# Optimization experiments

Hardware: AMD Instinct MI355X
Metric: run time of the kernel (lower is better)

Reference implementation:

```python
import jax, jax.numpy as jnp
import numpy as np
import math

B, N = 16, 32            # batch, num_agents
D_OBS = 128              # obs_input_dim
N_ACT = 16               # num_actions
D_OA_IN = D_OBS + N_ACT  # obs_act_input_dim = 144
D_OUT = 128              # obs_output_dim == obs_act_output_dim
HID = 64                 # final hidden
FINAL_OUT = 1


def _xavier(k, shape):
    fan_out, fan_in = shape
    lim = math.sqrt(6.0 / (fan_in + fan_out))
    return jax.random.uniform(k, shape, jnp.float32, -lim, lim)


def setup_inputs() -> dict:
    key = jax.random.key(0)
    ks = jax.random.split(key, 12)
    return {
        "states": jax.random.normal(ks[0], (B, N, D_OBS), jnp.float32),
        "policies": jax.random.uniform(ks[1], (B, N, N_ACT), jnp.float32),
        "actions": jax.random.uniform(ks[2], (B, N, N_ACT), jnp.float32),
        # uniform noise in [0,1); forward applies (noise-0.5)*0.1 like torch.rand path
        "noise": jax.random.uniform(ks[3], (B, N, N, N, D_OUT), jnp.float32),
        # torch Linear weights: [out_features, in_features], bias=False
        "Wk_oa": _xavier(ks[4], (D_OUT, D_OA_IN)),
        "Wq_oa": _xavier(ks[5], (D_OUT, D_OA_IN)),
        "Wv_oa": _xavier(ks[6], (D_OUT, D_OA_IN)),
        "Wk_o": _xavier(ks[7], (D_OUT, D_OBS)),
        "Wq_o": _xavier(ks[8], (D_OUT, D_OBS)),
        "Wv_o": _xavier(ks[9], (D_OUT, D_OBS)),
        "W1": _xavier(ks[10], (HID, 2 * D_OUT)),
        "W2": _xavier(ks[11], (FINAL_OUT, HID)),
    }


def reference(states, policies, actions, noise, Wk_oa, Wq_oa, Wv_oa, Wk_o, Wq_o, Wv_o, W1, W2):
    n = states.shape[1]
    d_oa = Wk_oa.shape[0]
    d_o = Wk_o.shape[0]

    obs_actions = jnp.concatenate([states, actions], axis=-1)   # [B,N,D_oa_in]
    obs_policy = jnp.concatenate([states, policies], axis=-1)

    # --- obs-action attention branch ---
    K = obs_actions @ Wk_oa.T                                   # [B,N,d]
    Q = obs_actions @ Wq_oa.T
    # bmm(Q,K^T).transpose(1,2): score_t[b,j,i] = Q_i . K_j; softmax over i
    score_t = jnp.einsum('bid,bjd->bji', Q, K)
    w_oa = jax.nn.softmax(score_t / jnp.sqrt(jnp.asarray(d_oa, states.dtype)), axis=-1)  # [B,N,N]

    # place_policies/place_actions: diagonal picks obs_policy, off-diag obs_actions
    eye = jnp.eye(n, dtype=states.dtype)[None, :, :, None]       # [1,N,N,1]
    oap = eye * obs_policy[:, None, :, :] + (1.0 - eye) * obs_actions[:, None, :, :]  # [B,N,N,D_oa_in]
    AV = oap @ Wv_oa.T                                           # [B,N,N,d]

    # mean_i( AV[b,j,i,:] * w_oa[b,k,i] + (noise-0.5)*0.1 ); mean is linear -> split
    noise_mean = jnp.mean((noise - 0.5) * 0.1, axis=-2)          # [B,N,N,d]
    wav = jnp.einsum('bjid,bki->bkjd', AV, w_oa) / n + noise_mean  # [B,N,N,d]

    # --- obs-only attention branch ---
    Ko = states @ Wk_o.T
    Qo = states @ Wq_o.T
    AVO = states @ Wv_o.T                                        # [B,N,d]
    score_o = jnp.einsum('bid,bjd->bji', Qo, Ko)
    w_o = jax.nn.softmax(score_o / jnp.sqrt(jnp.asarray(d_o, states.dtype)), axis=-1)  # [B,N,N]
    wfo = jnp.einsum('bji,bid->bjd', w_o, AVO) / n               # [B,N,d]
    wfo_b = jnp.broadcast_to(wfo[:, :, None, :], wav.shape[:3] + (d_o,))  # [B,N,N,d]

    node = jnp.concatenate([wfo_b, wav], axis=-1)                # [B,N,N,2d]
    h = jax.nn.leaky_relu(node @ W1.T, negative_slope=0.01)
    value = h @ W2.T                                             # [B,N,N,1]
    return (value, w_oa, w_o[..., None])
```

## Files before the change

### kernel.cpp

```cpp
#include <hip/hip_runtime.h>


#define WS_K    0
#define WS_Q    65536
#define WS_VA   131072
#define WS_KO   196608
#define WS_QO   262144
#define WS_AVO  327680
#define WS_SDIV 393216
#define WS_DDIV 458752
#define WS_U    524288
#define WS_WOA  557056

__global__ __launch_bounds__(256) void k_transforms(
    const float* __restrict__ states, const float* __restrict__ policies,
    const float* __restrict__ actions,
    const float* __restrict__ Wk_oa, const float* __restrict__ Wq_oa,
    const float* __restrict__ Wv_oa, const float* __restrict__ Wk_o,
    const float* __restrict__ Wq_o,  const float* __restrict__ Wv_o,
    float* __restrict__ ws)
{
    __shared__ __align__(16) float xa[144];
    const int row = blockIdx.x;
    const int t = threadIdx.x;
    if (t < 128)       xa[t] = states[row * 128 + t];
    else if (t < 144)  xa[t] = actions[row * 16 + (t - 128)];
    __syncthreads();

    for (int u = t; u < 768; u += 256) {
        const int m = u >> 7, o = u & 127;
        const float* Wrow; int len4; float* dst;
        switch (m) {
            case 0: Wrow = Wk_oa + o * 144; len4 = 36; dst = ws + WS_K;  break;
            case 1: Wrow = Wq_oa + o * 144; len4 = 36; dst = ws + WS_Q;  break;
            case 2: Wrow = Wv_oa + o * 144; len4 = 36; dst = ws + WS_VA; break;
            case 3: Wrow = Wk_o  + o * 128; len4 = 32; dst = ws + WS_KO; break;
            case 4: Wrow = Wq_o  + o * 128; len4 = 32; dst = ws + WS_QO; break;
            default:Wrow = Wv_o  + o * 128; len4 = 32; dst = ws + WS_AVO;break;
        }
        const float4* W4 = (const float4*)Wrow;
        const float4* x4 = (const float4*)xa;
        float acc = 0.f;
        for (int c = 0; c < len4; ++c) {
            float4 w = W4[c], x = x4[c];
            acc += w.x * x.x + w.y * x.y + w.z * x.z + w.w * x.w;
        }
        dst[row * 128 + o] = acc;
    }
}

__global__ __launch_bounds__(256) void k_attn(
    const float* __restrict__ policies, const float* __restrict__ actions,
    const float* __restrict__ Wv_oa, const float* __restrict__ W1,
    float* __restrict__ ws, float* __restrict__ out)
{
    const float* K   = ws + WS_K;
    const float* Q   = ws + WS_Q;
    const float* Va  = ws + WS_VA;
    const float* Ko  = ws + WS_KO;
    const float* Qo  = ws + WS_QO;
    const float* AVO = ws + WS_AVO;
    float* Sdiv = ws + WS_SDIV;
    float* Ddiv = ws + WS_DDIV;
    float* U    = ws + WS_U;
    float* Woa  = ws + WS_WOA;

    const int b = blockIdx.x >> 5, r = blockIdx.x & 31;
    const int t = threadIdx.x;
    const int br = b * 32 + r;

    __shared__ __align__(16) float kr[128], kor[128], wfo[128];
    __shared__ float sA[32], sO[32], woa[32], wo[32], pd[16];

    if (t < 128) { kr[t] = K[br * 128 + t]; kor[t] = Ko[br * 128 + t]; }
    else if (t < 144) {
        int c = t - 128;
        pd[c] = policies[br * 16 + c] - actions[br * 16 + c];
    }
    __syncthreads();

    {
        const int i = t >> 3, seg = t & 7;
        const float4* q4  = (const float4*)(Q  + (b * 32 + i) * 128) + seg * 4;
        const float4* qo4 = (const float4*)(Qo + (b * 32 + i) * 128) + seg * 4;
        const float4* k4  = (const float4*)kr  + seg * 4;
        const float4* ko4 = (const float4*)kor + seg * 4;
        float a0 = 0.f, a1 = 0.f;
        #pragma unroll
        for (int c = 0; c < 4; ++c) {
            float4 q = q4[c], kk = k4[c];
            a0 += q.x * kk.x + q.y * kk.y + q.z * kk.z + q.w * kk.w;
            float4 p = qo4[c], mm = ko4[c];
            a1 += p.x * mm.x + p.y * mm.y + p.z * mm.z + p.w * mm.w;
        }
        #pragma unroll
        for (int off = 1; off < 8; off <<= 1) {
            a0 += __shfl_xor(a0, off, 64);
            a1 += __shfl_xor(a1, off, 64);
        }
        if (seg == 0) {
            const float scale = 0.08838834764831845f;
            sA[i] = a0 * scale;
            sO[i] = a1 * scale;
        }
    }
    __syncthreads();

    if (t < 64) {
        const int i = t & 31;
        float s = (t < 32) ? sA[i] : sO[i];
        float m = s;
        #pragma unroll
        for (int off = 1; off < 32; off <<= 1) m = fmaxf(m, __shfl_xor(m, off, 64));
        float e = __expf(s - m);
        float sum = e;
        #pragma unroll
        for (int off = 1; off < 32; off <<= 1) sum += __shfl_xor(sum, off, 64);
        float w = e / sum;
        if (t < 32) { woa[i] = w; out[16384 + br * 32 + i] = w; Woa[br * 32 + i] = w; }
        else        { wo[i]  = w; out[32768 + br * 32 + i] = w; }
    }
    __syncthreads();

    {
        const int d = t & 127;
        const float* M  = (t < 128) ? Va  : AVO;
        const float* wp = (t < 128) ? woa : wo;
        float acc = 0.f;
        #pragma unroll 8
        for (int i = 0; i < 32; ++i) acc += wp[i] * M[(b * 32 + i) * 128 + d];
        if (t < 128) {
            Sdiv[br * 128 + d] = acc * (1.f / 32.f);
            const float4* wv4 = (const float4*)(Wv_oa + d * 144 + 128);
            float dv = 0.f;
            #pragma unroll
            for (int c = 0; c < 4; ++c) {
                float4 w = wv4[c];
                dv += w.x * pd[4*c] + w.y * pd[4*c+1] + w.z * pd[4*c+2] + w.w * pd[4*c+3];
            }
            Ddiv[br * 128 + d] = dv * (1.f / 32.f);
        } else {
            wfo[d] = acc * (1.f / 32.f);
        }
    }
    __syncthreads();

    {
        const int h = t >> 2, q = t & 3;
        const float4* w4 = (const float4*)(W1 + h * 256) + q * 8;
        const float4* f4 = (const float4*)wfo + q * 8;
        float acc = 0.f;
        #pragma unroll
        for (int c = 0; c < 8; ++c) {
            float4 w = w4[c], f = f4[c];
            acc += w.x * f.x + w.y * f.y + w.z * f.z + w.w * f.w;
        }
        acc += __shfl_xor(acc, 1, 64);
        acc += __shfl_xor(acc, 2, 64);
        if (q == 0) U[br * 64 + h] = acc;
    }
}

__global__ __launch_bounds__(256) void k_value(
    const float* __restrict__ noise, const float* __restrict__ ws,
    const float* __restrict__ W1, const float* __restrict__ W2,
    float* __restrict__ out)
{
    const float* Sdiv = ws + WS_SDIV;
    const float* Ddiv = ws + WS_DDIV;
    const float* U    = ws + WS_U;
    const float* Woa  = ws + WS_WOA;

    const int blk = blockIdx.x;
    const int b  = blk >> 6;
    const int k  = (blk >> 1) & 31;
    const int j0 = (blk & 1) * 16;
    const int t  = threadIdx.x;
    const int h  = t >> 2, q = t & 3;
    const int lane = t & 63, wv = t >> 6;
    const int bk = b * 32 + k;

    __shared__ __align__(16) float part[512];
    __shared__ __align__(16) float wav_s[4 * 36];
    __shared__ float sdiv_s[128];
    __shared__ float woa_s[16];
    __shared__ float wsum[4];

    float w1r[32];
    {
        const float4* p = (const float4*)(W1 + h * 256 + 128 + q * 32);
        #pragma unroll
        for (int c = 0; c < 8; ++c) {
            float4 v = p[c];
            w1r[4*c] = v.x; w1r[4*c+1] = v.y; w1r[4*c+2] = v.z; w1r[4*c+3] = v.w;
        }
    }
    const float u_h  = U[bk * 64 + h];
    const float w2_h = W2[h];
    if (t < 128) sdiv_s[t] = Sdiv[bk * 128 + t];
    if (t < 16)  woa_s[t]  = Woa[bk * 32 + j0 + t];
    __syncthreads();

    const float4* nbase = (const float4*)noise + (size_t)(bk * 32) * 1024;

    float4 n0, n1, n2, n3;
    {
        const float4* p = nbase + (size_t)j0 * 1024 + t;
        n0 = p[0]; n1 = p[256]; n2 = p[512]; n3 = p[768];
    }
    for (int jj = 0; jj < 16; ++jj) {
        const int j = j0 + jj;
        float4 m0{}, m1{}, m2{}, m3{};
        if (jj < 15) {
            const float4* p = nbase + (size_t)(j + 1) * 1024 + t;
            m0 = p[0]; m1 = p[256]; m2 = p[512]; m3 = p[768];
        }
        float s0 = n0.x + n1.x + n2.x + n3.x;
        float s1 = n0.y + n1.y + n2.y + n3.y;
        float s2 = n0.z + n1.z + n2.z + n3.z;
        float s3 = n0.w + n1.w + n2.w + n3.w;
        s0 += __shfl_xor(s0, 32, 64);
        s1 += __shfl_xor(s1, 32, 64);
        s2 += __shfl_xor(s2, 32, 64);
        s3 += __shfl_xor(s3, 32, 64);
        if (lane < 32) {
            float4 v; v.x = s0; v.y = s1; v.z = s2; v.w = s3;
            ((float4*)part)[wv * 32 + lane] = v;
        }
        __syncthreads();
        if (t < 128) {
            float ns = part[t] + part[128 + t] + part[256 + t] + part[384 + t];
            float dv = Ddiv[(b * 32 + j) * 128 + t];
            float w  = sdiv_s[t] + dv * woa_s[jj] + ns * (0.1f / 32.f) - 0.05f;
            wav_s[(t >> 5) * 36 + (t & 31)] = w;
        }
        __syncthreads();
        {
            const float4* wv4 = (const float4*)(wav_s + q * 36);
            float acc = 0.f;
            #pragma unroll
            for (int c = 0; c < 8; ++c) {
                float4 v = wv4[c];
                acc += w1r[4*c] * v.x + w1r[4*c+1] * v.y
                     + w1r[4*c+2] * v.z + w1r[4*c+3] * v.w;
            }
            acc += __shfl_xor(acc, 1, 64);
            acc += __shfl_xor(acc, 2, 64);
            float hv = u_h + acc;
            hv = (hv > 0.f) ? hv : 0.01f * hv;
            float vp = (q == 0) ? hv * w2_h : 0.f;
            #pragma unroll
            for (int off = 4; off < 64; off <<= 1) vp += __shfl_xor(vp, off, 64);
            if (lane == 0) wsum[wv] = vp;
        }
        __syncthreads();
        if (t == 0) out[bk * 32 + j] = wsum[0] + wsum[1] + wsum[2] + wsum[3];
        n0 = m0; n1 = m1; n2 = m2; n3 = m3;
    }
}

extern "C" void kernel_launch(void* const* d_in, const int* in_sizes, int n_in,
                              void* d_out, int out_size, void* d_ws, size_t ws_size,
                              hipStream_t stream) {
    const float* states   = (const float*)d_in[0];
    const float* policies = (const float*)d_in[1];
    const float* actions  = (const float*)d_in[2];
    const float* noise    = (const float*)d_in[3];
    const float* Wk_oa    = (const float*)d_in[4];
    const float* Wq_oa    = (const float*)d_in[5];
    const float* Wv_oa    = (const float*)d_in[6];
    const float* Wk_o     = (const float*)d_in[7];
    const float* Wq_o     = (const float*)d_in[8];
    const float* Wv_o     = (const float*)d_in[9];
    const float* W1       = (const float*)d_in[10];
    const float* W2       = (const float*)d_in[11];
    float* out = (float*)d_out;
    float* ws  = (float*)d_ws;

    k_transforms<<<512, 256, 0, stream>>>(states, policies, actions,
                                          Wk_oa, Wq_oa, Wv_oa, Wk_o, Wq_o, Wv_o, ws);
    k_attn<<<512, 256, 0, stream>>>(policies, actions, Wv_oa, W1, ws, out);
    k_value<<<1024, 256, 0, stream>>>(noise, ws, W1, W2, out);
}
```

Before: 416.6 us.

## Fold noise reduction into transform kernel and fuse attention with value head

The three-kernel pipeline becomes two. The first kernel runs the linear transforms, including the policy-action diagonal correction, and also reduces the noise tensor over its reduction axis with many independent loads in flight, writing the partial sums to workspace. The second kernel fuses attention, softmax and the value MLP per (b,k) row and stages the Ddiv and noise sums in shared memory, which removes the per-j sync-heavy loop. The aim is to cut a launch and the serialized noise streaming. The cost is about 32KB of shared memory per block in kB, which may reduce occupancy.

```diff
diff --git a/kernel.cpp b/kernel.cpp
--- a/kernel.cpp
+++ b/kernel.cpp
@@ -7,76 +7,136 @@
 #define WS_KO   196608
 #define WS_QO   262144
 #define WS_AVO  327680
-#define WS_SDIV 393216
-#define WS_DDIV 458752
-#define WS_U    524288
-#define WS_WOA  557056
-
-__global__ __launch_bounds__(256) void k_transforms(
+#define WS_DDIV 393216
+#define WS_NSUM 458752
+
+__global__ __launch_bounds__(256) void kA(
     const float* __restrict__ states, const float* __restrict__ policies,
     const float* __restrict__ actions,
     const float* __restrict__ Wk_oa, const float* __restrict__ Wq_oa,
     const float* __restrict__ Wv_oa, const float* __restrict__ Wk_o,
     const float* __restrict__ Wq_o,  const float* __restrict__ Wv_o,
-    float* __restrict__ ws)
+    const float* __restrict__ noise, float* __restrict__ ws)
 {
-    __shared__ __align__(16) float xa[144];
-    const int row = blockIdx.x;
-    const int t = threadIdx.x;
-    if (t < 128)       xa[t] = states[row * 128 + t];
-    else if (t < 144)  xa[t] = actions[row * 16 + (t - 128)];
-    __syncthreads();
-
-    for (int u = t; u < 768; u += 256) {
-        const int m = u >> 7, o = u & 127;
-        const float* Wrow; int len4; float* dst;
-        switch (m) {
-            case 0: Wrow = Wk_oa + o * 144; len4 = 36; dst = ws + WS_K;  break;
-            case 1: Wrow = Wq_oa + o * 144; len4 = 36; dst = ws + WS_Q;  break;
-            case 2: Wrow = Wv_oa + o * 144; len4 = 36; dst = ws + WS_VA; break;
-            case 3: Wrow = Wk_o  + o * 128; len4 = 32; dst = ws + WS_KO; break;
-            case 4: Wrow = Wq_o  + o * 128; len4 = 32; dst = ws + WS_QO; break;
-            default:Wrow = Wv_o  + o * 128; len4 = 32; dst = ws + WS_AVO;break;
-        }
-        const float4* W4 = (const float4*)Wrow;
-        const float4* x4 = (const float4*)xa;
-        float acc = 0.f;
-        for (int c = 0; c < len4; ++c) {
-            float4 w = W4[c], x = x4[c];
-            acc += w.x * x.x + w.y * x.y + w.z * x.z + w.w * x.w;
-        }
-        dst[row * 128 + o] = acc;
+    const int t   = threadIdx.x;
+    const int blk = blockIdx.x;
+
+    __shared__ __align__(16) float xa[160];
+
+    if (blk < 512) {
+        const int row = blk;
+        if (t < 128)       xa[t] = states[row * 128 + t];
+        else if (t < 144)  xa[t] = actions[row * 16 + (t - 128)];
+        else if (t < 160) {
+            int c = t - 144;
+            xa[t] = policies[row * 16 + c] - actions[row * 16 + c];
+        }
+        __syncthreads();
+
+        for (int u = t; u < 896; u += 256) {
+            const int m = u >> 7, o = u & 127;
+            const float* Wrow; int len4; float* dst; const float* xsrc = xa;
+            switch (m) {
+                case 0: Wrow = Wk_oa + o * 144; len4 = 36; dst = ws + WS_K;  break;
+                case 1: Wrow = Wq_oa + o * 144; len4 = 36; dst = ws + WS_Q;  break;
+                case 2: Wrow = Wv_oa + o * 144; len4 = 36; dst = ws + WS_VA; break;
+                case 3: Wrow = Wk_o  + o * 128; len4 = 32; dst = ws + WS_KO; break;
+                case 4: Wrow = Wq_o  + o * 128; len4 = 32; dst = ws + WS_QO; break;
+                case 5: Wrow = Wv_o  + o * 128; len4 = 32; dst = ws + WS_AVO;break;
+                default:Wrow = Wv_oa + o * 144 + 128; len4 = 4;
+                        dst = ws + WS_DDIV; xsrc = xa + 144; break;
+            }
+            const float4* W4 = (const float4*)Wrow;
+            const float4* x4 = (const float4*)xsrc;
+            float acc = 0.f;
+            for (int c = 0; c < len4; ++c) {
+                float4 w = W4[c], x = x4[c];
+                acc += w.x * x.x + w.y * x.y + w.z * x.z + w.w * x.w;
+            }
+            dst[row * 128 + o] = (m == 6) ? acc * (1.f / 32.f) : acc;
+        }
+    }
+
+    const int bk   = blk >> 1;
+    const int j0   = (blk & 1) * 16;
+    const int w    = t >> 6, lane = t & 63;
+    const float4* noise4 = (const float4*)noise;
+    float4* nsum4 = (float4*)(ws + WS_NSUM);
+
+    #pragma unroll
+    for (int s = 0; s < 4; ++s) {
+        const int j = j0 + 4 * s + w;
+        const float4* p = noise4 + (size_t)(bk * 32 + j) * 1024 + lane;
+        float4 a0 = p[0], a1 = p[64], a2 = p[128], a3 = p[192];
+        #pragma unroll
+        for (int r = 4; r < 16; r += 4) {
+            float4 v0 = p[(r + 0) * 64], v1 = p[(r + 1) * 64];
+            float4 v2 = p[(r + 2) * 64], v3 = p[(r + 3) * 64];
+            a0.x += v0.x; a0.y += v0.y; a0.z += v0.z; a0.w += v0.w;
+            a1.x += v1.x; a1.y += v1.y; a1.z += v1.z; a1.w += v1.w;
+            a2.x += v2.x; a2.y += v2.y; a2.z += v2.z; a2.w += v2.w;
+            a3.x += v3.x; a3.y += v3.y; a3.z += v3.z; a3.w += v3.w;
+        }
+        float4 sum;
+        sum.x = (a0.x + a1.x) + (a2.x + a3.x);
+        sum.y = (a0.y + a1.y) + (a2.y + a3.y);
+        sum.z = (a0.z + a1.z) + (a2.z + a3.z);
+        sum.w = (a0.w + a1.w) + (a2.w + a3.w);
+        sum.x += __shfl_xor(sum.x, 32, 64);
+        sum.y += __shfl_xor(sum.y, 32, 64);
+        sum.z += __shfl_xor(sum.z, 32, 64);
+        sum.w += __shfl_xor(sum.w, 32, 64);
+        if (lane < 32) nsum4[(size_t)(bk * 32 + j) * 32 + lane] = sum;
     }
 }
 
-__global__ __launch_bounds__(256) void k_attn(
-    const float* __restrict__ policies, const float* __restrict__ actions,
-    const float* __restrict__ Wv_oa, const float* __restrict__ W1,
-    float* __restrict__ ws, float* __restrict__ out)
+__global__ __launch_bounds__(256) void kB(
+    const float* __restrict__ W1, const float* __restrict__ W2,
+    const float* __restrict__ ws, float* __restrict__ out)
 {
-    const float* K   = ws + WS_K;
+    const float* Kk  = ws + WS_K;
     const float* Q   = ws + WS_Q;
     const float* Va  = ws + WS_VA;
     const float* Ko  = ws + WS_KO;
     const float* Qo  = ws + WS_QO;
     const float* AVO = ws + WS_AVO;
-    float* Sdiv = ws + WS_SDIV;
-    float* Ddiv = ws + WS_DDIV;
-    float* U    = ws + WS_U;
-    float* Woa  = ws + WS_WOA;
-
-    const int b = blockIdx.x >> 5, r = blockIdx.x & 31;
-    const int t = threadIdx.x;
-    const int br = b * 32 + r;
-
-    __shared__ __align__(16) float kr[128], kor[128], wfo[128];
-    __shared__ float sA[32], sO[32], woa[32], wo[32], pd[16];
-
-    if (t < 128) { kr[t] = K[br * 128 + t]; kor[t] = Ko[br * 128 + t]; }
-    else if (t < 144) {
-        int c = t - 128;
-        pd[c] = policies[br * 16 + c] - actions[br * 16 + c];
-    }
+    const float* Ddiv= ws + WS_DDIV;
+    const float* Nsum= ws + WS_NSUM;
+
+    const int bk = blockIdx.x;
+    const int b  = bk >> 5;
+    const int t  = threadIdx.x;
+    const int h  = t >> 2, q = t & 3;
+    const int lane = t & 63, w = t >> 6;
+
+    __shared__ __align__(16) float kr[128], kor[128], wfo[128], sdiv[128];
+    __shared__ __align__(16) float dd_s[32 * 128];
+    __shared__ __align__(16) float nw_s[32 * 128];
+    __shared__ float sA[32], sO[32], woa[32], wo[32], u_s[64], jpart[128];
+
+    {
+        const float4* dsrc = (const float4*)(Ddiv + b * 4096);
+        const float4* nsrc = (const float4*)(Nsum + (size_t)bk * 4096);
+        float4* ddst = (float4*)dd_s;
+        float4* ndst = (float4*)nw_s;
+        #pragma unroll
+        for (int s = 0; s < 4; ++s) {
+            ddst[t + 256 * s] = dsrc[t + 256 * s];
+            ndst[t + 256 * s] = nsrc[t + 256 * s];
+        }
+    }
+    if (t < 128) { kr[t] = Kk[bk * 128 + t]; kor[t] = Ko[bk * 128 + t]; }
+
+    float w1r[32];
+    {
+        const float4* p = (const float4*)(W1 + h * 256 + 128 + q * 32);
+        #pragma unroll
+        for (int c = 0; c < 8; ++c) {
+            float4 v = p[c];
+            w1r[4*c] = v.x; w1r[4*c+1] = v.y; w1r[4*c+2] = v.z; w1r[4*c+3] = v.w;
+        }
+    }
+    const float w2_h = W2[h];
     __syncthreads();
 
     {
@@ -88,10 +148,10 @@
         float a0 = 0.f, a1 = 0.f;
         #pragma unroll
         for (int c = 0; c < 4; ++c) {
-            float4 q = q4[c], kk = k4[c];
-            a0 += q.x * kk.x + q.y * kk.y + q.z * kk.z + q.w * kk.w;
-            float4 p = qo4[c], mm = ko4[c];
-            a1 += p.x * mm.x + p.y * mm.y + p.z * mm.z + p.w * mm.w;
+            float4 qv = q4[c], kv = k4[c];
+            a0 += qv.x * kv.x + qv.y * kv.y + qv.z * kv.z + qv.w * kv.w;
+            float4 pv = qo4[c], mv = ko4[c];
+            a1 += pv.x * mv.x + pv.y * mv.y + pv.z * mv.z + pv.w * mv.w;
         }
         #pragma unroll
         for (int off = 1; off < 8; off <<= 1) {
@@ -116,9 +176,9 @@
         float sum = e;
         #pragma unroll
         for (int off = 1; off < 32; off <<= 1) sum += __shfl_xor(sum, off, 64);
-        float w = e / sum;
-        if (t < 32) { woa[i] = w; out[16384 + br * 32 + i] = w; Woa[br * 32 + i] = w; }
-        else        { wo[i]  = w; out[32768 + br * 32 + i] = w; }
+        float wv = e / sum;
+        if (t < 32) { woa[i] = wv; out[16384 + bk * 32 + i] = wv; }
+        else        { wo[i]  = wv; out[32768 + bk * 32 + i] = wv; }
     }
     __syncthreads();
 
@@ -129,134 +189,57 @@
         float acc = 0.f;
         #pragma unroll 8
         for (int i = 0; i < 32; ++i) acc += wp[i] * M[(b * 32 + i) * 128 + d];
-        if (t < 128) {
-            Sdiv[br * 128 + d] = acc * (1.f / 32.f);
-            const float4* wv4 = (const float4*)(Wv_oa + d * 144 + 128);
-            float dv = 0.f;
-            #pragma unroll
-            for (int c = 0; c < 4; ++c) {
-                float4 w = wv4[c];
-                dv += w.x * pd[4*c] + w.y * pd[4*c+1] + w.z * pd[4*c+2] + w.w * pd[4*c+3];
-            }
-            Ddiv[br * 128 + d] = dv * (1.f / 32.f);
-        } else {
-            wfo[d] = acc * (1.f / 32.f);
-        }
-    }
-    __syncthreads();
-
-    {
-        const int h = t >> 2, q = t & 3;
+        if (t < 128) sdiv[d] = acc * (1.f / 32.f);
+        else         wfo[d]  = acc * (1.f / 32.f);
+    }
+    __syncthreads();
+
+    {
         const float4* w4 = (const float4*)(W1 + h * 256) + q * 8;
         const float4* f4 = (const float4*)wfo + q * 8;
         float acc = 0.f;
         #pragma unroll
         for (int c = 0; c < 8; ++c) {
-            float4 w = w4[c], f = f4[c];
-            acc += w.x * f.x + w.y * f.y + w.z * f.z + w.w * f.w;
+            float4 wv = w4[c], fv = f4[c];
+            acc += wv.x * fv.x + wv.y * fv.y + wv.z * fv.z + wv.w * fv.w;
         }
         acc += __shfl_xor(acc, 1, 64);
         acc += __shfl_xor(acc, 2, 64);
-        if (q == 0) U[br * 64 + h] = acc;
-    }
-}
-
-__global__ __launch_bounds__(256) void k_value(
-    const float* __restrict__ noise, const float* __restrict__ ws,
-    const float* __restrict__ W1, const float* __restrict__ W2,
-    float* __restrict__ out)
-{
-    const float* Sdiv = ws + WS_SDIV;
-    const float* Ddiv = ws + WS_DDIV;
-    const float* U    = ws + WS_U;
-    const float* Woa  = ws + WS_WOA;
-
-    const int blk = blockIdx.x;
-    const int b  = blk >> 6;
-    const int k  = (blk >> 1) & 31;
-    const int j0 = (blk & 1) * 16;
-    const int t  = threadIdx.x;
-    const int h  = t >> 2, q = t & 3;
-    const int lane = t & 63, wv = t >> 6;
-    const int bk = b * 32 + k;
-
-    __shared__ __align__(16) float part[512];
-    __shared__ __align__(16) float wav_s[4 * 36];
-    __shared__ float sdiv_s[128];
-    __shared__ float woa_s[16];
-    __shared__ float wsum[4];
-
-    float w1r[32];
-    {
-        const float4* p = (const float4*)(W1 + h * 256 + 128 + q * 32);
+        if (q == 0) u_s[h] = acc;
+    }
+    {
+        const int d = t & 127, jb = t >> 7;
+        #pragma unroll
+        for (int s = 0; s < 16; ++s) {
+            const int j = jb + 2 * s;
+            nw_s[j * 128 + d] = nw_s[j * 128 + d] * (0.1f / 32.f)
+                              + sdiv[d] + dd_s[j * 128 + d] * woa[j] - 0.05f;
+        }
+    }
+    __syncthreads();
+
+    #pragma unroll 2
+    for (int j = 0; j < 32; ++j) {
+        const float4* wv4 = (const float4*)(nw_s + j * 128 + q * 32);
+        float acc = 0.f;
         #pragma unroll
         for (int c = 0; c < 8; ++c) {
-            float4 v = p[c];
-            w1r[4*c] = v.x; w1r[4*c+1] = v.y; w1r[4*c+2] = v.z; w1r[4*c+3] = v.w;
-        }
-    }
-    const float u_h  = U[bk * 64 + h];
-    const float w2_h = W2[h];
-    if (t < 128) sdiv_s[t] = Sdiv[bk * 128 + t];
-    if (t < 16)  woa_s[t]  = Woa[bk * 32 + j0 + t];
-    __syncthreads();
-
-    const float4* nbase = (const float4*)noise + (size_t)(bk * 32) * 1024;
-
-    float4 n0, n1, n2, n3;
-    {
-        const float4* p = nbase + (size_t)j0 * 1024 + t;
-        n0 = p[0]; n1 = p[256]; n2 = p[512]; n3 = p[768];
-    }
-    for (int jj = 0; jj < 16; ++jj) {
-        const int j = j0 + jj;
-        float4 m0{}, m1{}, m2{}, m3{};
-        if (jj < 15) {
-            const float4* p = nbase + (size_t)(j + 1) * 1024 + t;
-            m0 = p[0]; m1 = p[256]; m2 = p[512]; m3 = p[768];
-        }
-        float s0 = n0.x + n1.x + n2.x + n3.x;
-        float s1 = n0.y + n1.y + n2.y + n3.y;
-        float s2 = n0.z + n1.z + n2.z + n3.z;
-        float s3 = n0.w + n1.w + n2.w + n3.w;
-        s0 += __shfl_xor(s0, 32, 64);
-        s1 += __shfl_xor(s1, 32, 64);
-        s2 += __shfl_xor(s2, 32, 64);
-        s3 += __shfl_xor(s3, 32, 64);
-        if (lane < 32) {
-            float4 v; v.x = s0; v.y = s1; v.z = s2; v.w = s3;
-            ((float4*)part)[wv * 32 + lane] = v;
-        }
-        __syncthreads();
-        if (t < 128) {
-            float ns = part[t] + part[128 + t] + part[256 + t] + part[384 + t];
-            float dv = Ddiv[(b * 32 + j) * 128 + t];
-            float w  = sdiv_s[t] + dv * woa_s[jj] + ns * (0.1f / 32.f) - 0.05f;
-            wav_s[(t >> 5) * 36 + (t & 31)] = w;
-        }
-        __syncthreads();
-        {
-            const float4* wv4 = (const float4*)(wav_s + q * 36);
-            float acc = 0.f;
-            #pragma unroll
-            for (int c = 0; c < 8; ++c) {
-                float4 v = wv4[c];
-                acc += w1r[4*c] * v.x + w1r[4*c+1] * v.y
-                     + w1r[4*c+2] * v.z + w1r[4*c+3] * v.w;
-            }
-            acc += __shfl_xor(acc, 1, 64);
-            acc += __shfl_xor(acc, 2, 64);
-            float hv = u_h + acc;
-            hv = (hv > 0.f) ? hv : 0.01f * hv;
-            float vp = (q == 0) ? hv * w2_h : 0.f;
-            #pragma unroll
-            for (int off = 4; off < 64; off <<= 1) vp += __shfl_xor(vp, off, 64);
-            if (lane == 0) wsum[wv] = vp;
-        }
-        __syncthreads();
-        if (t == 0) out[bk * 32 + j] = wsum[0] + wsum[1] + wsum[2] + wsum[3];
-        n0 = m0; n1 = m1; n2 = m2; n3 = m3;
-    }
+            float4 v = wv4[c];
+            acc += w1r[4*c] * v.x + w1r[4*c+1] * v.y
+                 + w1r[4*c+2] * v.z + w1r[4*c+3] * v.w;
+        }
+        acc += __shfl_xor(acc, 1, 64);
+        acc += __shfl_xor(acc, 2, 64);
+        float hv = u_s[h] + acc;
+        hv = (hv > 0.f) ? hv : 0.01f * hv;
+        float vp = (q == 0) ? hv * w2_h : 0.f;
+        #pragma unroll
+        for (int off = 4; off < 64; off <<= 1) vp += __shfl_xor(vp, off, 64);
+        if (lane == 0) jpart[j * 4 + w] = vp;
+    }
+    __syncthreads();
+    if (t < 32)
+        out[bk * 32 + t] = jpart[t*4] + jpart[t*4+1] + jpart[t*4+2] + jpart[t*4+3];
 }
 
 extern "C" void kernel_launch(void* const* d_in, const int* in_sizes, int n_in,
@@ -277,8 +260,8 @@
     float* out = (float*)d_out;
     float* ws  = (float*)d_ws;
 
-    k_transforms<<<512, 256, 0, stream>>>(states, policies, actions,
-                                          Wk_oa, Wq_oa, Wv_oa, Wk_o, Wq_o, Wv_o, ws);
-    k_attn<<<512, 256, 0, stream>>>(policies, actions, Wv_oa, W1, ws, out);
-    k_value<<<1024, 256, 0, stream>>>(noise, ws, W1, W2, out);
+    kA<<<1024, 256, 0, stream>>>(states, policies, actions,
+                                 Wk_oa, Wq_oa, Wv_oa, Wk_o, Wq_o, Wv_o,
+                                 noise, ws);
+    kB<<<512, 256, 0, stream>>>(W1, W2, ws, out);
 }
```

Result: slower. 425.3 us (+2.1%).
